# Optimization experiments

Hardware: AMD Instinct MI355X
Metric: run time of the kernel (lower is better)

Reference implementation:

```python
import math
import jax, jax.numpy as jnp
import numpy as np

B, N = 1, 512
C_S, C_Z, H, C, P_Q, P_V = 384, 128, 12, 16, 4, 8
CAT = C_Z * H + C * H + 3 * H * P_V + 1  # 2017


def _apply(t_r, t_t, x):
    # t_r: (b,n,3,3), t_t: (b,n,3), x: (b,3,h,p,n) -> global frame coords
    xg = jnp.einsum('bnij,bjhpn->bihpn', t_r, x)
    return xg + jnp.swapaxes(t_t, 1, 2)[:, :, None, None, :]


def setup_inputs() -> dict:
    key = jax.random.key(0)
    ks = jax.random.split(key, 14)
    f = lambda k, shp: jax.random.normal(k, shp, dtype=jnp.float32)
    return {
        's': f(ks[0], (B, C_S, N)),
        'z': f(ks[1], (B, C_Z, N, N)),
        't_r': f(ks[2], (B, N, 3, 3)),
        't_t': f(ks[3], (B, N, 3)),
        'Wq': f(ks[4], (C * H, C_S)) * 0.02,
        'Wk': f(ks[5], (C * H, C_S)) * 0.02,
        'Wv': f(ks[6], (C * H, C_S)) * 0.02,
        'Wqp': f(ks[7], (3 * H * P_Q, C_S)) * 0.02,
        'Wkp': f(ks[8], (3 * H * P_Q, C_S)) * 0.02,
        'Wvp': f(ks[9], (3 * H * P_V, C_S)) * 0.02,
        'Wb': f(ks[10], (H, C_Z)) * 0.02,
        'gamma': f(ks[11], (H, 1, 1)) * 0.5,
        'Ws': f(ks[12], (C_S, CAT)) * 0.02,
        'bs': jnp.zeros((C_S,), dtype=jnp.float32),
    }


def reference(s, z, t_r, t_t, Wq, Wk, Wv, Wqp, Wkp, Wvp, Wb, gamma, Ws, bs):
    b, _, n = s.shape
    w_c = math.sqrt(2.0 / (9.0 * P_Q))
    w_l = math.sqrt(1.0 / 3.0)

    proj = lambda W: jnp.einsum('oc,bcn->bon', W, s)
    # torch rearrange 'b (c h) i -> b c h i' == reshape(b, c, h, n)
    q = proj(Wq).reshape(b, C, H, n)
    k = proj(Wk).reshape(b, C, H, n)
    v = proj(Wv).reshape(b, C, H, n)
    qp = proj(Wqp).reshape(b, 3, H, P_Q, n)
    kp = proj(Wkp).reshape(b, 3, H, P_Q, n)
    vp = proj(Wvp).reshape(b, 3, H, P_V, n)

    qg = _apply(t_r, t_t, qp)  # (b,3,h,p,n)
    kg = _apply(t_r, t_t, kp)
    diff = qg[..., :, None] - kg[..., None, :]          # (b,3,h,p,n,n)
    dist2 = jnp.sum(diff * diff, axis=(1, 3))           # sum coords + points -> (b,h,n,n)
    tmp = jax.nn.softplus(gamma)[None] * (w_c / 2.0) * dist2

    b_bias = jnp.einsum('hc,bcij->bhij', Wb, z)
    qk = jnp.einsum('bchi,bchj->bhij', q, k) / math.sqrt(C)
    a = jax.nn.softmax(w_l * (qk + b_bias - tmp), axis=-1)  # (b,h,n,n)

    o1 = jnp.einsum('bhij,bcij->bchi', a, z).reshape(b, C_Z * H, n)
    o2 = jnp.einsum('bhij,bchj->bchi', a, v).reshape(b, C * H, n)

    vg = _apply(t_r, t_t, vp)                           # (b,3,h,pv,n)
    o3g = jnp.einsum('bhij,bchpj->bchpi', a, vg)        # (b,3,h,pv,n)
    t_r_inv = jnp.swapaxes(t_r, -1, -2)
    t_t_inv = jnp.einsum('bnij,bnj->bni', -t_r_inv, t_t)
    o3 = _apply(t_r_inv, t_t_inv, o3g).reshape(b, 3 * H * P_V, n)
    o3_norm = jnp.linalg.norm(o3, axis=1, keepdims=True)  # (b,1,n)

    cat = jnp.concatenate([o1, o2, o3, o3_norm], axis=1)  # (b, CAT, n)
    return jnp.einsum('oc,bcn->bon', Ws, cat) + bs[None, :, None]
```

## Files before the change

### kernel.cpp

```cpp
#include <hip/hip_runtime.h>
#include <math.h>

#define N 512
#define H 12
#define CC 16
#define CZ 128
#define CS 384
#define PQ 4
#define PV 8
#define CATR 2017

__global__ __launch_bounds__(256) void k_proj(
    const float* __restrict__ s,
    const float* __restrict__ Wq, const float* __restrict__ Wk, const float* __restrict__ Wv,
    const float* __restrict__ Wqp, const float* __restrict__ Wkp, const float* __restrict__ Wvp,
    float* __restrict__ proj)
{
    __shared__ float Wt[16][33];
    __shared__ float St[32][128];
    int t = threadIdx.x;
    int o0 = blockIdx.x * 16;
    int n0 = blockIdx.y * 128;
    const float* Wsrc; int orow;
    if (o0 < 192)      { Wsrc = Wq;  orow = o0; }
    else if (o0 < 384) { Wsrc = Wk;  orow = o0-192; }
    else if (o0 < 576) { Wsrc = Wv;  orow = o0-384; }
    else if (o0 < 720) { Wsrc = Wqp; orow = o0-576; }
    else if (o0 < 864) { Wsrc = Wkp; orow = o0-720; }
    else               { Wsrc = Wvp; orow = o0-864; }

    int og = t >> 6, nl = t & 63;
    float acc[4][2] = {};
    for (int c0 = 0; c0 < CS; c0 += 32) {
        __syncthreads();
        for (int k = 0; k < 2; k++) {
            int idx = t + k*256;
            int oo = idx >> 5, ccol = idx & 31;
            Wt[oo][ccol] = Wsrc[(orow+oo)*CS + c0 + ccol];
        }
        for (int k = 0; k < 4; k++) {
            int idx = t + k*256;
            int ccr = idx >> 5, nn4 = idx & 31;
            float4 v = *(const float4*)&s[(c0+ccr)*N + n0 + nn4*4];
            *(float4*)&St[ccr][nn4*4] = v;
        }
        __syncthreads();
        for (int kk = 0; kk < 32; kk++) {
            float sv0 = St[kk][nl], sv1 = St[kk][nl+64];
            #pragma unroll
            for (int r = 0; r < 4; r++) {
                float w = Wt[og*4+r][kk];
                acc[r][0] += w * sv0;
                acc[r][1] += w * sv1;
            }
        }
    }
    float scale = (o0 < 192) ? 0.25f : 1.0f;
    for (int r = 0; r < 4; r++) {
        int o = o0 + og*4 + r;
        proj[o*N + n0 + nl]      = scale * acc[r][0];
        proj[o*N + n0 + 64 + nl] = scale * acc[r][1];
    }
}

__global__ void k_frames(const float* __restrict__ proj,
                         const float* __restrict__ t_r, const float* __restrict__ t_t,
                         float* __restrict__ qg, float* __restrict__ kg, float* __restrict__ vg)
{
    int gid = blockIdx.x * blockDim.x + threadIdx.x;
    int n = gid & (N-1);
    int hp = gid >> 9;
    if (hp >= 192) return;
    const float* src; float* dst; int rowb, stride;
    if (hp < 48)      { src = proj + 576*N; dst = qg; rowb = hp;    stride = 48; }
    else if (hp < 96) { src = proj + 720*N; dst = kg; rowb = hp-48; stride = 48; }
    else              { src = proj + 864*N; dst = vg; rowb = hp-96; stride = 96; }
    float x0 = src[(rowb + 0*stride)*N + n];
    float x1 = src[(rowb + 1*stride)*N + n];
    float x2 = src[(rowb + 2*stride)*N + n];
    #pragma unroll
    for (int d = 0; d < 3; d++) {
        float r0 = t_r[(n*3+d)*3+0], r1 = t_r[(n*3+d)*3+1], r2 = t_r[(n*3+d)*3+2];
        dst[(rowb + d*stride)*N + n] = r0*x0 + r1*x1 + r2*x2 + t_t[n*3+d];
    }
}

__global__ __launch_bounds__(256) void k_qkgeom(
    const float* __restrict__ proj, const float* __restrict__ qg,
    const float* __restrict__ kg, const float* __restrict__ gamma,
    float* __restrict__ a)
{
    __shared__ float Qe[30][32];
    __shared__ float Ke[30][128];
    const int h  = blockIdx.x;
    const int i0 = blockIdx.y * 32;
    const int j0 = blockIdx.z * 128;
    const int t  = threadIdx.x;
    const float w_c2 = 0.11785113019775793f;
    float g = gamma[h];
    float sp = (g > 20.f) ? g : log1pf(expf(g));
    float ch = sp * w_c2;

    for (int idx = t; idx < 28*32; idx += 256) {
        int row = idx >> 5, col = idx & 31;
        float v;
        if (row < 16) v = proj[(size_t)(row*12 + h)*N + i0 + col];
        else { int dp = row-16, d = dp>>2, p = dp&3;
               v = 2.f*ch * qg[(size_t)(d*48 + h*4 + p)*N + i0 + col]; }
        Qe[row][col] = v;
    }
    for (int idx = t; idx < 28*128; idx += 256) {
        int row = idx >> 7, col = idx & 127;
        float v;
        if (row < 16) v = proj[(size_t)((192 + row*12 + h))*N + j0 + col];
        else { int dp = row-16, d = dp>>2, p = dp&3;
               v = kg[(size_t)(d*48 + h*4 + p)*N + j0 + col]; }
        Ke[row][col] = v;
    }
    if (t < 32) {
        float q2 = 0.f;
        #pragma unroll
        for (int dp = 0; dp < 12; ++dp) {
            int d = dp>>2, p = dp&3;
            float v = qg[(size_t)(d*48 + h*4 + p)*N + i0 + t];
            q2 = fmaf(v, v, q2);
        }
        Qe[28][t] = 1.f;
        Qe[29][t] = -ch * q2;
    } else if (t < 160) {
        int col = t - 32;
        float k2 = 0.f;
        #pragma unroll
        for (int dp = 0; dp < 12; ++dp) {
            int d = dp>>2, p = dp&3;
            float v = kg[(size_t)(d*48 + h*4 + p)*N + j0 + col];
            k2 = fmaf(v, v, k2);
        }
        Ke[28][col] = -ch * k2;
        Ke[29][col] = 1.f;
    }
    __syncthreads();

    const int tj = t & 31, ti = t >> 5;
    float acc[4][4] = {};
    #pragma unroll
    for (int c = 0; c < 30; ++c) {
        float4 k4 = *(const float4*)&Ke[c][tj*4];
        float4 q4 = *(const float4*)&Qe[c][ti*4];
        float qr[4] = {q4.x, q4.y, q4.z, q4.w};
        #pragma unroll
        for (int r = 0; r < 4; ++r) {
            acc[r][0] = fmaf(qr[r], k4.x, acc[r][0]);
            acc[r][1] = fmaf(qr[r], k4.y, acc[r][1]);
            acc[r][2] = fmaf(qr[r], k4.z, acc[r][2]);
            acc[r][3] = fmaf(qr[r], k4.w, acc[r][3]);
        }
    }
    #pragma unroll
    for (int r = 0; r < 4; ++r) {
        float4 v; v.x = acc[r][0]; v.y = acc[r][1]; v.z = acc[r][2]; v.w = acc[r][3];
        *(float4*)&a[((size_t)h*N + i0 + ti*4 + r)*N + j0 + tj*4] = v;
    }
}

__global__ __launch_bounds__(512) void k_logits2(
    const float* __restrict__ z, const float* __restrict__ Wb,
    float* __restrict__ a)
{
    __shared__ float zt[16*512];
    __shared__ float pm[12][8];
    __shared__ float ps[12][8];
    const int i = blockIdx.x;
    const int t = threadIdx.x;
    const int w = t >> 6;
    const int l = t & 63;
    const size_t NN = (size_t)N * N;
    const float w_l = 0.57735026918962584f;

    float acc[12];
    #pragma unroll
    for (int h = 0; h < 12; ++h)
        acc[h] = a[((size_t)h*N + i)*N + t];

    {
        const int zc = t >> 5;
        const int zj = (t & 31) * 4;
        const float* zsrc = z + (size_t)zc*NN + (size_t)i*N + zj;
        float4 g0 = *(const float4*)(zsrc);
        float4 g1 = *(const float4*)(zsrc + 128);
        float4 g2 = *(const float4*)(zsrc + 256);
        float4 g3 = *(const float4*)(zsrc + 384);
        *(float4*)&zt[zc*512 + zj]       = g0;
        *(float4*)&zt[zc*512 + zj + 128] = g1;
        *(float4*)&zt[zc*512 + zj + 256] = g2;
        *(float4*)&zt[zc*512 + zj + 384] = g3;
        __syncthreads();
        for (int tb = 0; tb < 8; ++tb) {
            if (tb < 7) {
                const float* zn = zsrc + (size_t)(tb+1)*16*NN;
                g0 = *(const float4*)(zn);
                g1 = *(const float4*)(zn + 128);
                g2 = *(const float4*)(zn + 256);
                g3 = *(const float4*)(zn + 384);
            }
            #pragma unroll
            for (int c = 0; c < 16; ++c) {
                float zv = zt[c*512 + t];
                #pragma unroll
                for (int h = 0; h < 12; ++h)
                    acc[h] = fmaf(Wb[h*CZ + tb*16 + c], zv, acc[h]);
            }
            __syncthreads();
            if (tb < 7) {
                *(float4*)&zt[zc*512 + zj]       = g0;
                *(float4*)&zt[zc*512 + zj + 128] = g1;
                *(float4*)&zt[zc*512 + zj + 256] = g2;
                *(float4*)&zt[zc*512 + zj + 384] = g3;
                __syncthreads();
            }
        }
    }

    float lv[12], mw[12];
    #pragma unroll
    for (int h = 0; h < 12; ++h)
        lv[h] = w_l * acc[h];

    #pragma unroll
    for (int h = 0; h < 12; ++h) {
        float m = lv[h];
        for (int s = 32; s; s >>= 1) m = fmaxf(m, __shfl_xor(m, s));
        float e = __expf(lv[h] - m);
        float sm = e;
        for (int s = 32; s; s >>= 1) sm += __shfl_xor(sm, s);
        lv[h] = e; mw[h] = m;
        if (l == 0) { pm[h][w] = m; ps[h][w] = sm; }
    }
    __syncthreads();
    #pragma unroll
    for (int h = 0; h < 12; ++h) {
        float mg = pm[h][0];
        #pragma unroll
        for (int u = 1; u < 8; ++u) mg = fmaxf(mg, pm[h][u]);
        float sg = 0.f;
        #pragma unroll
        for (int u = 0; u < 8; ++u) sg += ps[h][u] * __expf(pm[h][u] - mg);
        float f = __expf(mw[h] - mg) / sg;
        a[((size_t)h*N + i)*N + t] = lv[h] * f;
    }
}

__global__ __launch_bounds__(256, 8) void k_o1(
    const float* __restrict__ a, const float* __restrict__ z,
    float* __restrict__ o1T)
{
    __shared__ float zls[64*36];
    __shared__ float als[12][36];
    const int i  = blockIdx.x;
    const int c0 = blockIdx.y * 64;
    const int t  = threadIdx.x;
    const int cg = t & 31, hg = (t >> 5) & 1, jq = t >> 6;

    float acc[2][6] = {};
    for (int jc = 0; jc < 16; ++jc) {
        __syncthreads();
        #pragma unroll
        for (int k = 0; k < 2; ++k) {
            int idx = t + k*256;
            int c = idx >> 3, j4 = idx & 7;
            *(float4*)&zls[c*36 + j4*4] =
                *(const float4*)&z[((size_t)(c0+c)*N + i)*N + jc*32 + j4*4];
        }
        if (t < 96) {
            int h = t >> 3, j4 = t & 7;
            *(float4*)&als[h][j4*4] =
                *(const float4*)&a[((size_t)h*N + i)*N + jc*32 + j4*4];
        }
        __syncthreads();
        #pragma unroll
        for (int s = 0; s < 2; ++s) {
            int jo = jq*8 + s*4;
            float4 a4[6];
            #pragma unroll
            for (int hh = 0; hh < 6; ++hh)
                a4[hh] = *(const float4*)&als[hg*6+hh][jo];
            #pragma unroll
            for (int r = 0; r < 2; ++r) {
                float4 z4 = *(const float4*)&zls[(cg + 32*r)*36 + jo];
                #pragma unroll
                for (int hh = 0; hh < 6; ++hh)
                    acc[r][hh] += z4.x*a4[hh].x + z4.y*a4[hh].y
                                + z4.z*a4[hh].z + z4.w*a4[hh].w;
            }
        }
    }
    const int sl = t & 63;
    __syncthreads();
    if (jq >= 2) {
        float* rb = &zls[(jq-2)*832 + sl*13];
        #pragma unroll
        for (int r = 0; r < 2; ++r)
            #pragma unroll
            for (int hh = 0; hh < 6; ++hh) rb[r*6+hh] = acc[r][hh];
    }
    __syncthreads();
    if (jq < 2) {
        const float* rb = &zls[jq*832 + sl*13];
        #pragma unroll
        for (int r = 0; r < 2; ++r)
            #pragma unroll
            for (int hh = 0; hh < 6; ++hh) acc[r][hh] += rb[r*6+hh];
    }
    __syncthreads();
    if (jq == 1) {
        float* rb = &zls[sl*13];
        #pragma unroll
        for (int r = 0; r < 2; ++r)
            #pragma unroll
            for (int hh = 0; hh < 6; ++hh) rb[r*6+hh] = acc[r][hh];
    }
    __syncthreads();
    if (jq == 0) {
        const float* rb = &zls[sl*13];
        #pragma unroll
        for (int r = 0; r < 2; ++r)
            #pragma unroll
            for (int hh = 0; hh < 3; ++hh) {
                int c = c0 + cg + 32*r, h = hg*6 + hh*2;
                float2 v2;
                v2.x = acc[r][hh*2]   + rb[r*6+hh*2];
                v2.y = acc[r][hh*2+1] + rb[r*6+hh*2+1];
                *(float2*)&o1T[(size_t)i*1536 + c*12 + h] = v2;
            }
    }
}

__global__ __launch_bounds__(256) void k_o2o3g(
    const float* __restrict__ a, const float* __restrict__ proj, const float* __restrict__ vg,
    float* __restrict__ catB, float* __restrict__ o3g)
{
    __shared__ float ats[8*132];
    __shared__ float vts[40*132];
    int h = blockIdx.x, i0 = blockIdx.y*8;
    int t = threadIdx.x;
    int il = t & 7, rg = (t>>3)&7, jq = t>>6;
    const float* v = proj + 384*N;
    float acc[5] = {};
    for (int jc = 0; jc < 4; jc++) {
        __syncthreads();
        {
            int ii = t >> 5, j4 = t & 31;
            *(float4*)&ats[ii*132 + j4*4] =
                *(const float4*)&a[((size_t)h*N + i0+ii)*N + jc*128 + j4*4];
        }
        #pragma unroll
        for (int k = 0; k < 5; k++) {
            int idx = t + k*256;
            int r = idx >> 5, j4 = idx & 31;
            const float* src = (r < 16) ? (v + (size_t)(r*H + h)*N)
                : (vg + (size_t)(((r-16)>>3)*96 + h*PV + ((r-16)&7))*N);
            *(float4*)&vts[r*132 + j4*4] = *(const float4*)&src[jc*128 + j4*4];
        }
        __syncthreads();
        #pragma unroll
        for (int s = 0; s < 8; s++) {
            int jo = jq*32 + s*4;
            float4 a4 = *(const float4*)&ats[il*132 + jo];
            #pragma unroll
            for (int r = 0; r < 5; r++) {
                float4 v4 = *(const float4*)&vts[(rg*5+r)*132 + jo];
                acc[r] += v4.x*a4.x + v4.y*a4.y + v4.z*a4.z + v4.w*a4.w;
            }
        }
    }
    __syncthreads();
    if (jq >= 2) {
        float* rb = &ats[((jq-2)*64 + (t & 63))*5];
        #pragma unroll
        for (int r = 0; r < 5; r++) rb[r] = acc[r];
    }
    __syncthreads();
    if (jq < 2) {
        const float* rb = &ats[(jq*64 + (t & 63))*5];
        #pragma unroll
        for (int r = 0; r < 5; r++) acc[r] += rb[r];
        if (jq == 1) {
            float* rb2 = &ats[640 + (t & 63)*5];
            #pragma unroll
            for (int r = 0; r < 5; r++) rb2[r] = acc[r];
        }
    }
    __syncthreads();
    if (jq == 0) {
        const float* rb2 = &ats[640 + t*5];
        #pragma unroll
        for (int r = 0; r < 5; r++) {
            float val = acc[r] + rb2[r];
            int row = rg*5 + r;
            if (row < 16) catB[(size_t)(row*H + h)*N + i0 + il] = val;
            else { int rr = row - 16;
                   o3g[(size_t)((rr>>3)*96 + h*PV + (rr&7))*N + i0 + il] = val; }
        }
    }
}

__global__ void k_o3(const float* __restrict__ o3g,
                     const float* __restrict__ t_r, const float* __restrict__ t_t,
                     float* __restrict__ catB)
{
    int gid = blockIdx.x*blockDim.x + threadIdx.x;
    int i = gid & (N-1), hp = gid >> 9;
    if (hp >= 96) return;
    float x0 = o3g[(size_t)(0*96 + hp)*N + i] - t_t[i*3+0];
    float x1 = o3g[(size_t)(1*96 + hp)*N + i] - t_t[i*3+1];
    float x2 = o3g[(size_t)(2*96 + hp)*N + i] - t_t[i*3+2];
    #pragma unroll
    for (int d = 0; d < 3; d++) {
        float o = t_r[(i*3+0)*3+d]*x0 + t_r[(i*3+1)*3+d]*x1 + t_r[(i*3+2)*3+d]*x2;
        catB[(size_t)(192 + d*96 + hp)*N + i] = o;
    }
}

__global__ void k_norm(float* __restrict__ catB)
{
    __shared__ float red[8][32];
    int il = threadIdx.x & 31, g = threadIdx.x >> 5;
    int i = blockIdx.x*32 + il;
    float acc = 0.f;
    for (int r = g*36; r < g*36 + 36; ++r) {
        float v = catB[(size_t)(192+r)*N + i];
        acc += v*v;
    }
    red[g][il] = acc;
    __syncthreads();
    if (g == 0) {
        acc = 0.f;
        #pragma unroll
        for (int u = 0; u < 8; ++u) acc += red[u][il];
        catB[(size_t)480*N + i] = sqrtf(acc);
    }
}

__global__ __launch_bounds__(256) void k_final(
    const float* __restrict__ Ws, const float* __restrict__ bs,
    const float* __restrict__ o1T, const float* __restrict__ catB,
    float* __restrict__ out)
{
    __shared__ float Wt[16*33];
    __shared__ float Ct[32*66];
    int o0 = blockIdx.x*16, n0 = blockIdx.y*64;
    int ks = blockIdx.z;
    int kbeg = ks*512, kend = min(CATR, kbeg+512);
    int t = threadIdx.x;
    int og = t >> 6, nl = t & 63;
    float acc[4] = {};
    for (int c0 = kbeg; c0 < kend; c0 += 32) {
        __syncthreads();
        for (int k = 0; k < 2; k++) {
            int idx = t + k*256;
            int oo = idx >> 5, ccol = idx & 31;
            int c = c0 + ccol;
            Wt[oo*33 + ccol] = (c < kend) ? Ws[(size_t)(o0+oo)*CATR + c] : 0.f;
        }
        if (ks < 3) {
            for (int k = 0; k < 2; k++) {
                int idx = t + k*256;
                int nn = idx >> 3, c4 = idx & 7;
                float4 v = *(const float4*)&o1T[(size_t)(n0+nn)*1536 + c0 + c4*4];
                Ct[(c4*4+0)*66 + nn] = v.x;
                Ct[(c4*4+1)*66 + nn] = v.y;
                Ct[(c4*4+2)*66 + nn] = v.z;
                Ct[(c4*4+3)*66 + nn] = v.w;
            }
        } else {
            for (int k = 0; k < 4; k++) {
                int idx = t + k*256;
                int ccr = idx >> 5, j2 = idx & 31;
                int c = c0 + ccr;
                float2 vv; vv.x = 0.f; vv.y = 0.f;
                if (c < kend) vv = *(const float2*)&catB[(size_t)(c-1536)*N + n0 + j2*2];
                *(float2*)&Ct[ccr*66 + j2*2] = vv;
            }
        }
        __syncthreads();
        int klim = min(32, kend - c0);
        for (int kk = 0; kk < klim; kk++) {
            float cv = Ct[kk*66 + nl];
            #pragma unroll
            for (int r = 0; r < 4; r++)
                acc[r] += Wt[(og*4+r)*33 + kk] * cv;
        }
    }
    #pragma unroll
    for (int r = 0; r < 4; r++) {
        int o = o0 + og*4 + r;
        float val = acc[r];
        if (ks == 0) val += bs[o];
        atomicAdd(&out[(size_t)o*N + n0 + nl], val);
    }
}

extern "C" void kernel_launch(void* const* d_in, const int* in_sizes, int n_in,
                              void* d_out, int out_size, void* d_ws, size_t ws_size,
                              hipStream_t stream)
{
    const float* s     = (const float*)d_in[0];
    const float* z     = (const float*)d_in[1];
    const float* t_r   = (const float*)d_in[2];
    const float* t_t   = (const float*)d_in[3];
    const float* Wq    = (const float*)d_in[4];
    const float* Wk    = (const float*)d_in[5];
    const float* Wv    = (const float*)d_in[6];
    const float* Wqp   = (const float*)d_in[7];
    const float* Wkp   = (const float*)d_in[8];
    const float* Wvp   = (const float*)d_in[9];
    const float* Wb    = (const float*)d_in[10];
    const float* gamma = (const float*)d_in[11];
    const float* Ws    = (const float*)d_in[12];
    const float* bs    = (const float*)d_in[13];
    float* out = (float*)d_out;

    float* ws   = (float*)d_ws;
    float* proj = ws;
    float* qg   = proj + 1152*N;
    float* kg   = qg   + 144*N;
    float* vg   = kg   + 144*N;
    float* o3g  = vg   + 288*N;
    float* a    = o3g  + 288*N;
    float* o1T  = a    + (size_t)H*N*N;
    float* catB = o1T  + (size_t)N*1536;

    k_proj   <<<dim3(72,4),    256, 0, stream>>>(s, Wq, Wk, Wv, Wqp, Wkp, Wvp, proj);
    k_frames <<<384,           256, 0, stream>>>(proj, t_r, t_t, qg, kg, vg);
    k_qkgeom <<<dim3(12,16,4), 256, 0, stream>>>(proj, qg, kg, gamma, a);
    k_logits2<<<512,           512, 0, stream>>>(z, Wb, a);
    k_o1     <<<dim3(512,2),   256, 0, stream>>>(a, z, o1T);
    k_o2o3g  <<<dim3(12,64),   256, 0, stream>>>(a, proj, vg, catB, o3g);
    k_o3     <<<192,           256, 0, stream>>>(o3g, t_r, t_t, catB);
    k_norm   <<<16,            256, 0, stream>>>(catB);
    hipMemsetAsync(out, 0, (size_t)CS*N*sizeof(float), stream);
    k_final  <<<dim3(24,8,4),  256, 0, stream>>>(Ws, bs, o1T, catB, out);
}
```

Before: 375.9 us.

## Split z-bias accumulation from softmax into a more parallel kernel

Splits the fused logits kernel into two. k_zbias runs on a 512x8 grid: each block covers 64 columns, splits the 128 z channels across four waves, and combines the partial sums through shared memory. A separate softmax kernel then reads the updated logits. This is meant to expose more parallelism and memory-level concurrency for the large z read, at the cost of an extra launch and a full read-modify-write pass over the 12x512x512 logits tensor.

Result: slower. 410.2 us (+9.1%).

```diff
diff --git a/kernel.cpp b/kernel.cpp
--- a/kernel.cpp
+++ b/kernel.cpp
@@ -163,68 +163,64 @@
     }
 }
 
-__global__ __launch_bounds__(512) void k_logits2(
+__global__ __launch_bounds__(256) void k_zbias(
     const float* __restrict__ z, const float* __restrict__ Wb,
     float* __restrict__ a)
 {
-    __shared__ float zt[16*512];
+    __shared__ float red[3*832];
+    const int i  = blockIdx.x;
+    const int j0 = blockIdx.y * 64;
+    const int t  = threadIdx.x;
+    const int jl = t & 63, cg = t >> 6;
+    const size_t NN = (size_t)N * N;
+
+    const float* zp = z + (size_t)(cg*32)*NN + (size_t)i*N + j0 + jl;
+    float acc[12] = {};
+    for (int cc = 0; cc < 32; cc += 16) {
+        float zb[16];
+        #pragma unroll
+        for (int u = 0; u < 16; ++u) zb[u] = zp[(size_t)(cc+u)*NN];
+        #pragma unroll
+        for (int h = 0; h < 12; ++h)
+            #pragma unroll
+            for (int u = 0; u < 16; ++u)
+                acc[h] = fmaf(Wb[h*CZ + cg*32 + cc + u], zb[u], acc[h]);
+    }
+    if (cg > 0) {
+        float* rb = &red[(cg-1)*832 + jl*13];
+        #pragma unroll
+        for (int h = 0; h < 12; ++h) rb[h] = acc[h];
+    }
+    __syncthreads();
+    if (cg == 0) {
+        #pragma unroll
+        for (int sl = 0; sl < 3; ++sl) {
+            const float* rb = &red[sl*832 + jl*13];
+            #pragma unroll
+            for (int h = 0; h < 12; ++h) acc[h] += rb[h];
+        }
+        #pragma unroll
+        for (int h = 0; h < 12; ++h) {
+            size_t idx = ((size_t)h*N + i)*N + j0 + jl;
+            a[idx] = a[idx] + acc[h];
+        }
+    }
+}
+
+__global__ __launch_bounds__(512) void k_softmax(float* __restrict__ a)
+{
     __shared__ float pm[12][8];
     __shared__ float ps[12][8];
     const int i = blockIdx.x;
     const int t = threadIdx.x;
     const int w = t >> 6;
     const int l = t & 63;
-    const size_t NN = (size_t)N * N;
     const float w_l = 0.57735026918962584f;
 
-    float acc[12];
+    float lv[12], mw[12];
     #pragma unroll
     for (int h = 0; h < 12; ++h)
-        acc[h] = a[((size_t)h*N + i)*N + t];
-
-    {
-        const int zc = t >> 5;
-        const int zj = (t & 31) * 4;
-        const float* zsrc = z + (size_t)zc*NN + (size_t)i*N + zj;
-        float4 g0 = *(const float4*)(zsrc);
-        float4 g1 = *(const float4*)(zsrc + 128);
-        float4 g2 = *(const float4*)(zsrc + 256);
-        float4 g3 = *(const float4*)(zsrc + 384);
-        *(float4*)&zt[zc*512 + zj]       = g0;
-        *(float4*)&zt[zc*512 + zj + 128] = g1;
-        *(float4*)&zt[zc*512 + zj + 256] = g2;
-        *(float4*)&zt[zc*512 + zj + 384] = g3;
-        __syncthreads();
-        for (int tb = 0; tb < 8; ++tb) {
-            if (tb < 7) {
-                const float* zn = zsrc + (size_t)(tb+1)*16*NN;
-                g0 = *(const float4*)(zn);
-                g1 = *(const float4*)(zn + 128);
-                g2 = *(const float4*)(zn + 256);
-                g3 = *(const float4*)(zn + 384);
-            }
-            #pragma unroll
-            for (int c = 0; c < 16; ++c) {
-                float zv = zt[c*512 + t];
-                #pragma unroll
-                for (int h = 0; h < 12; ++h)
-                    acc[h] = fmaf(Wb[h*CZ + tb*16 + c], zv, acc[h]);
-            }
-            __syncthreads();
-            if (tb < 7) {
-                *(float4*)&zt[zc*512 + zj]       = g0;
-                *(float4*)&zt[zc*512 + zj + 128] = g1;
-                *(float4*)&zt[zc*512 + zj + 256] = g2;
-                *(float4*)&zt[zc*512 + zj + 384] = g3;
-                __syncthreads();
-            }
-        }
-    }
-
-    float lv[12], mw[12];
-    #pragma unroll
-    for (int h = 0; h < 12; ++h)
-        lv[h] = w_l * acc[h];
+        lv[h] = w_l * a[((size_t)h*N + i)*N + t];
 
     #pragma unroll
     for (int h = 0; h < 12; ++h) {
@@ -533,7 +529,8 @@
     k_proj   <<<dim3(72,4),    256, 0, stream>>>(s, Wq, Wk, Wv, Wqp, Wkp, Wvp, proj);
     k_frames <<<384,           256, 0, stream>>>(proj, t_r, t_t, qg, kg, vg);
     k_qkgeom <<<dim3(12,16,4), 256, 0, stream>>>(proj, qg, kg, gamma, a);
-    k_logits2<<<512,           512, 0, stream>>>(z, Wb, a);
+    k_zbias  <<<dim3(512,8),   256, 0, stream>>>(z, Wb, a);
+    k_softmax<<<512,           512, 0, stream>>>(a);
     k_o1     <<<dim3(512,2),   256, 0, stream>>>(a, z, o1T);
     k_o2o3g  <<<dim3(12,64),   256, 0, stream>>>(a, proj, vg, catB, o3g);
     k_o3     <<<192,           256, 0, stream>>>(o3g, t_r, t_t, catB);
```
